# Kernel optimization log

Hardware: AMD Instinct MI355X
Metric: run time of the kernel (lower is better)

Reference implementation:

```python
import jax, jax.numpy as jnp
import numpy as np

B, T, D, U = 64, 512, 512, 512  # units must equal input feature dim (concat along axis -2)


def setup_inputs() -> dict:
    key = jax.random.key(0)
    ks = jax.random.split(key, 5)
    glorot = float(np.sqrt(2.0 / (D + U)))  # glorot_normal std
    x = jax.random.normal(ks[0], (B, T, D), dtype=jnp.float32)
    Wq = jax.random.normal(ks[1], (D, U), dtype=jnp.float32) * glorot
    Wk = jax.random.normal(ks[2], (D, U), dtype=jnp.float32) * glorot
    Wv = jax.random.normal(ks[3], (D, U), dtype=jnp.float32) * glorot
    Wrec = jax.random.normal(ks[4], (U, U), dtype=jnp.float32) * glorot
    return {"x": x, "Wq": Wq, "Wk": Wk, "Wv": Wv, "Wrec": Wrec}


def reference(x, Wq, Wk, Wv, Wrec):
    # Self_RNN forward (inference: dropout mask == ones).
    # Recurrent step over time:
    #   hist = h @ Wrec ; inp3 = stack([hist, prev_input, x_t]) -> (B,3,D)
    #   Q,K,V = inp3 @ {Wq,Wk,Wv}                              -> (B,3,U)
    #   keras batch_dot(key^T, query, axes=[1,2]) => scores[b,i,j] = K[b,i]·Q[b,j]
    #   softmax over j (the query axis); output row i=0 only:
    #   out = sum_j softmax_j(K[b,0]·Q[b,j]/sqrt(U)) * V[b,j]
    #   new states: (out, x_t).  K.rnn -> return last output.
    units = Wq.shape[1]
    scale = 1.0 / jnp.sqrt(jnp.asarray(units, x.dtype))

    def step(carry, x_t):
        h, prev = carry
        hist = h @ Wrec                               # (B,U)
        inp3 = jnp.stack([hist, prev, x_t], axis=1)   # (B,3,D)
        Q = inp3 @ Wq                                 # (B,3,U)
        K0 = inp3[:, 0] @ Wk                          # only key row 0 (hist) is used
        V = inp3 @ Wv                                 # (B,3,U)
        scores = jnp.einsum('bu,bju->bj', K0, Q) * scale   # (B,3)
        attn = jax.nn.softmax(scores, axis=-1)
        out = jnp.einsum('bj,bju->bu', attn, V)       # (B,U)
        return (out, x_t), None

    h0 = jnp.zeros((x.shape[0], units), x.dtype)
    p0 = jnp.zeros((x.shape[0], x.shape[-1]), x.dtype)
    (h_last, _), _ = jax.lax.scan(step, (h0, p0), jnp.swapaxes(x, 0, 1))
    return h_last
```

## Files before the change

### kernel.cpp

```cpp
#include <hip/hip_runtime.h>


typedef _Float16 f16;
typedef _Float16 half8 __attribute__((ext_vector_type(8)));
typedef _Float16 h2 __attribute__((ext_vector_type(2)));
typedef float floatx4 __attribute__((ext_vector_type(4)));
typedef unsigned long long u64;

#define AM_F32 0
#define AM_F16 1
#define BM_NN_F32 0
#define BM_BT_F16 1
#define BM_BT_F32 2

#if defined(__has_builtin)
#if __has_builtin(__builtin_amdgcn_fdot2)
#define HAS_FDOT2 1
#endif
#endif

__device__ inline float dot2f(h2 a, h2 b, float c) {
#ifdef HAS_FDOT2
  return __builtin_amdgcn_fdot2(a, b, c, false);
#else
  return c + (float)a[0] * (float)b[0] + (float)a[1] * (float)b[1];
#endif
}

template<int AMODE, int BMODE, int CT>
__global__ __launch_bounds__(256)
void gemm128(const void* __restrict__ Ap, const void* __restrict__ Bp,
             f16* __restrict__ C, int K, int ldbnn, long ldc, long coff,
             int ntiles) {
  __shared__ f16 Al[128 * 32];
  __shared__ f16 Bl[128 * 32];
  const int tid = threadIdx.x;
  const int lane = tid & 63;
  const int wid = tid >> 6;
  const int wr = wid >> 1, wc = wid & 1;
  const int mt = blockIdx.x / ntiles, nt = blockIdx.x % ntiles;
  const long m0 = (long)mt * 128, n0 = (long)nt * 128;

  floatx4 acc[4][4];
#pragma unroll
  for (int m = 0; m < 4; ++m)
#pragma unroll
    for (int n = 0; n < 4; ++n) acc[m][n] = (floatx4){0.f, 0.f, 0.f, 0.f};

  for (int k0 = 0; k0 < K; k0 += 32) {
    __syncthreads();
#pragma unroll
    for (int i = 0; i < 2; ++i) {
      const int slot = i * 256 + tid;
      const int row = slot >> 2;
      const int kc = (slot & 3) * 8;
      if constexpr (AMODE == AM_F16) {
        const f16* Ag = (const f16*)Ap;
        half8 v = *(const half8*)(Ag + (m0 + row) * (long)K + k0 + kc);
        *(half8*)(Al + slot * 8) = v;
      } else {
        const float* Ag = (const float*)Ap;
        const float* p = Ag + (m0 + row) * (long)K + k0 + kc;
        float4 v0 = *(const float4*)(p);
        float4 v1 = *(const float4*)(p + 4);
        half8 h;
        h[0] = (f16)v0.x; h[1] = (f16)v0.y; h[2] = (f16)v0.z; h[3] = (f16)v0.w;
        h[4] = (f16)v1.x; h[5] = (f16)v1.y; h[6] = (f16)v1.z; h[7] = (f16)v1.w;
        *(half8*)(Al + slot * 8) = h;
      }
    }
    if constexpr (BMODE == BM_NN_F32) {
      const float* Bg = (const float*)Bp;
      const int nn = tid & 127;
      const int kh = (tid >> 7) * 16;
#pragma unroll
      for (int j = 0; j < 16; j += 2) {
        float b0 = Bg[(long)(k0 + kh + j) * ldbnn + n0 + nn];
        float b1 = Bg[(long)(k0 + kh + j + 1) * ldbnn + n0 + nn];
        h2 hv; hv[0] = (f16)b0; hv[1] = (f16)b1;
        *(h2*)(Bl + nn * 32 + kh + j) = hv;
      }
    } else {
#pragma unroll
      for (int i = 0; i < 2; ++i) {
        const int slot = i * 256 + tid;
        const int row = slot >> 2;
        const int kc = (slot & 3) * 8;
        if constexpr (BMODE == BM_BT_F16) {
          const f16* Bg = (const f16*)Bp;
          half8 v = *(const half8*)(Bg + (n0 + row) * (long)K + k0 + kc);
          *(half8*)(Bl + slot * 8) = v;
        } else {
          const float* Bg = (const float*)Bp;
          const float* p = Bg + (n0 + row) * (long)K + k0 + kc;
          float4 v0 = *(const float4*)(p);
          float4 v1 = *(const float4*)(p + 4);
          half8 h;
          h[0] = (f16)v0.x; h[1] = (f16)v0.y; h[2] = (f16)v0.z; h[3] = (f16)v0.w;
          h[4] = (f16)v1.x; h[5] = (f16)v1.y; h[6] = (f16)v1.z; h[7] = (f16)v1.w;
          *(half8*)(Bl + slot * 8) = h;
        }
      }
    }
    __syncthreads();
    const int frow = lane & 15;
    const int fkc = (lane >> 4) * 8;
    half8 af[4], bf[4];
#pragma unroll
    for (int m = 0; m < 4; ++m)
      af[m] = *(const half8*)(Al + (wr * 64 + m * 16 + frow) * 32 + fkc);
#pragma unroll
    for (int n = 0; n < 4; ++n)
      bf[n] = *(const half8*)(Bl + (wc * 64 + n * 16 + frow) * 32 + fkc);
#pragma unroll
    for (int m = 0; m < 4; ++m)
#pragma unroll
      for (int n = 0; n < 4; ++n)
        acc[m][n] = __builtin_amdgcn_mfma_f32_16x16x32_f16(af[m], bf[n],
                                                           acc[m][n], 0, 0, 0);
  }
  const int crow = (lane >> 4) * 4;
  const int ccol = lane & 15;
#pragma unroll
  for (int m = 0; m < 4; ++m)
#pragma unroll
    for (int n = 0; n < 4; ++n)
#pragma unroll
      for (int r = 0; r < 4; ++r) {
        long row = m0 + wr * 64 + m * 16 + crow + r;
        long col = n0 + wc * 64 + n * 16 + ccol;
        if constexpr (CT)
          C[(coff + col) * ldc + row] = (f16)acc[m][n][r];
        else
          C[row * ldc + coff + col] = (f16)acc[m][n][r];
      }
}

__global__ void zero_ybuf(u64* ybuf) {
  ybuf[(size_t)blockIdx.x * 256 + threadIdx.x] = 0ull;
}

__global__ __launch_bounds__(256, 1)
void seq_kernel(const f16* __restrict__ Wt, const f16* __restrict__ GXV,
                u64* __restrict__ ybuf, float* __restrict__ out) {
  const int wg = blockIdx.x;
  const int grp = wg & 15;
  const int s = wg >> 4;
  const int tid = threadIdx.x;
  const int T = 512;

  __shared__ __align__(16) char wlds[64 * 1024];
  __shared__ float yred[16][4][68];
  __shared__ h2 hpk[4][256];
  __shared__ float swred[4][8];
  __shared__ float svals[4];

  {
    const int r = tid >> 2;
    const int cb = (tid & 3) * 256;
    const unsigned key = ((unsigned)(r >> 2) & 7u) << 4;
    const f16* src = Wt + (size_t)(s * 64 + r) * 512;
#pragma unroll
    for (int k = 0; k < 16; ++k) {
      half8 v = *(const half8*)((const char*)src + cb + k * 16);
      *(half8*)(wlds + r * 1024 + ((unsigned)(cb + k * 16) ^ key)) = v;
    }
  }
  {
    h2 z; z[0] = (f16)0.f; z[1] = (f16)0.f;
#pragma unroll
    for (int ch = 0; ch < 4; ++ch) hpk[ch][tid] = z;
  }
  __syncthreads();

  const int cg = tid & 15;
  const int p = tid >> 4;
  const unsigned cgx = ((unsigned)cg & 7u) << 4;
  const float scale = 0.04419417382415922f;
  const bool isV = (s < 8);
  u64* const yV = ybuf;
  u64* const s0p = ybuf + 65536;

  for (int t = 0; t < T; ++t) {
    const int par = t & 1;
    const u64 tagw = ((u64)(unsigned)(t + 1)) << 32;

    h2 gc4[4], gp4[4], xc4[4], xp4[4];
#pragma unroll
    for (int ch = 0; ch < 4; ++ch) {
      const f16* rowc = GXV + (((size_t)grp * 4 + ch) * T + t) * 1024;
      gc4[ch] = *(const h2*)(rowc + 2 * tid);
      xc4[ch] = *(const h2*)(rowc + 512 + 2 * tid);
      h2 z; z[0] = (f16)0.f; z[1] = (f16)0.f;
      gp4[ch] = z; xp4[ch] = z;
      if (t > 0) {
        gp4[ch] = *(const h2*)(rowc - 1024 + 2 * tid);
        xp4[ch] = *(const h2*)(rowc - 512 + 2 * tid);
      }
    }

    half8 ha[4][4];
#pragma unroll
    for (int g = 0; g < 4; ++g)
#pragma unroll
      for (int k4 = 0; k4 < 4; ++k4)
        ha[g][k4] = *(const half8*)&hpk[g][p * 16 + k4 * 4];
    float acc[4][4];
#pragma unroll
    for (int j = 0; j < 4; ++j)
#pragma unroll
      for (int g = 0; g < 4; ++g) acc[j][g] = 0.f;
#pragma unroll
    for (int j = 0; j < 4; ++j) {
      const char* rowb = wlds + (cg * 4 + j) * 1024;
#pragma unroll
      for (int k4 = 0; k4 < 4; ++k4) {
        half8 w = *(const half8*)(rowb + ((unsigned)(p * 64 + k4 * 16) ^ cgx));
#pragma unroll
        for (int e = 0; e < 4; ++e) {
          h2 wp; wp[0] = w[2 * e]; wp[1] = w[2 * e + 1];
#pragma unroll
          for (int g = 0; g < 4; ++g) {
            h2 hp; hp[0] = ha[g][k4][2 * e]; hp[1] = ha[g][k4][2 * e + 1];
            acc[j][g] = dot2f(wp, hp, acc[j][g]);
          }
        }
      }
    }
#pragma unroll
    for (int j = 0; j < 4; ++j)
#pragma unroll
      for (int g = 0; g < 4; ++g) yred[p][g][cg * 4 + j] = acc[j][g];
    __syncthreads();

    {
      const int ch = tid >> 6, c = tid & 63;
      float sum = 0.f;
#pragma unroll
      for (int p16 = 0; p16 < 16; ++p16) sum += yred[p16][ch][c];
      if (isV) {
        u64* dst = yV + (((size_t)grp * 2 + par) * 4 + ch) * 512 + s * 64 + c;
        __hip_atomic_store(dst, tagw | (u64)__float_as_uint(sum),
                           __ATOMIC_RELAXED, __HIP_MEMORY_SCOPE_AGENT);
      } else {
        const int u = (s - 8) * 64 + c;
        h2 hu = hpk[ch][u >> 1];
        float p0 = sum * (float)hu[u & 1];
#pragma unroll
        for (int off = 32; off > 0; off >>= 1) p0 += __shfl_down(p0, off);
        if (c == 0) {
          u64* dst = s0p + (((size_t)grp * 2 + par) * 4 + ch) * 8 + (s - 8);
          __hip_atomic_store(dst, tagw | (u64)__float_as_uint(p0),
                             __ATOMIC_RELAXED, __HIP_MEMORY_SCOPE_AGENT);
        }
      }
    }

    {
      float pr[8];
#pragma unroll
      for (int ch = 0; ch < 4; ++ch) {
        h2 hv = hpk[ch][tid];
        pr[2 * ch] = (float)gp4[ch][0] * (float)hv[0] +
                     (float)gp4[ch][1] * (float)hv[1];
        pr[2 * ch + 1] = (float)gc4[ch][0] * (float)hv[0] +
                         (float)gc4[ch][1] * (float)hv[1];
      }
#pragma unroll
      for (int off = 32; off > 0; off >>= 1)
#pragma unroll
        for (int i = 0; i < 8; ++i) pr[i] += __shfl_down(pr[i], off);
      if ((tid & 63) == 0) {
#pragma unroll
        for (int i = 0; i < 8; ++i) swred[tid >> 6][i] = pr[i];
      }
    }

    const u64* yb = yV + (((size_t)grp * 2 + par) * 4) * 512;
    const u64* s0a = s0p + (((size_t)grp * 2 + par) * 4 + ((tid >> 3) & 3)) * 8 +
                     (tid & 7);
    u64 wv[8];
    u64 w8 = tagw;
    for (;;) {
      bool ok = true;
#pragma unroll
      for (int ch = 0; ch < 4; ++ch) {
        wv[2 * ch] = __hip_atomic_load(yb + ch * 512 + 2 * tid,
                                       __ATOMIC_RELAXED, __HIP_MEMORY_SCOPE_AGENT);
        wv[2 * ch + 1] = __hip_atomic_load(yb + ch * 512 + 2 * tid + 1,
                                           __ATOMIC_RELAXED, __HIP_MEMORY_SCOPE_AGENT);
        ok = ok && (wv[2 * ch] >= tagw) && (wv[2 * ch + 1] >= tagw);
      }
      if (tid < 32) {
        w8 = __hip_atomic_load(s0a, __ATOMIC_RELAXED, __HIP_MEMORY_SCOPE_AGENT);
        ok = ok && (w8 >= tagw);
      }
      if (ok) break;
      __builtin_amdgcn_s_sleep(1);
    }

    if (tid < 32) {
      float sp = __uint_as_float((unsigned)w8);
      sp += __shfl_xor(sp, 1);
      sp += __shfl_xor(sp, 2);
      sp += __shfl_xor(sp, 4);
      if ((tid & 7) == 0) svals[tid >> 3] = sp;
    }
    __syncthreads();

#pragma unroll
    for (int ch = 0; ch < 4; ++ch) {
      float s0 = svals[ch] * scale;
      float s1 = (swred[0][2 * ch] + swred[1][2 * ch] + swred[2][2 * ch] +
                  swred[3][2 * ch]) * scale;
      float s2 = (swred[0][2 * ch + 1] + swred[1][2 * ch + 1] +
                  swred[2][2 * ch + 1] + swred[3][2 * ch + 1]) * scale;
      float mx = fmaxf(s0, fmaxf(s1, s2));
      float e0 = __expf(s0 - mx), e1 = __expf(s1 - mx), e2 = __expf(s2 - mx);
      float inv = 1.f / (e0 + e1 + e2);
      float a0 = e0 * inv, a1 = e1 * inv, a2 = e2 * inv;
      float v0 = __uint_as_float((unsigned)wv[2 * ch]);
      float v1 = __uint_as_float((unsigned)wv[2 * ch + 1]);
      float hn0 = a0 * v0 + a1 * (float)xp4[ch][0] + a2 * (float)xc4[ch][0];
      float hn1 = a0 * v1 + a1 * (float)xp4[ch][1] + a2 * (float)xc4[ch][1];
      h2 hn; hn[0] = (f16)hn0; hn[1] = (f16)hn1;
      hpk[ch][tid] = hn;
      if (t == T - 1 && s == 0) {
        out[((size_t)grp * 4 + ch) * 512 + 2 * tid] = hn0;
        out[((size_t)grp * 4 + ch) * 512 + 2 * tid + 1] = hn1;
      }
    }
    __syncthreads();
  }
}

extern "C" void kernel_launch(void* const* d_in, const int* in_sizes, int n_in,
                              void* d_out, int out_size, void* d_ws,
                              size_t ws_size, hipStream_t stream) {
  const float* x = (const float*)d_in[0];
  const float* Wq = (const float*)d_in[1];
  const float* Wk = (const float*)d_in[2];
  const float* Wv = (const float*)d_in[3];
  const float* Wrec = (const float*)d_in[4];
  float* out = (float*)d_out;

  char* ws = (char*)d_ws;
  f16* GXV = (f16*)ws;
  f16* Wt = (f16*)(ws + 67108864);
  f16* Wrk = (f16*)(ws + 68157440);
  f16* Wrq = (f16*)(ws + 68681728);
  f16* WgT = (f16*)(ws + 69206016);
  u64* ybuf = (u64*)(ws + 68681728);

  gemm128<AM_F32, BM_NN_F32, 0><<<16, 256, 0, stream>>>(Wrec, Wk, Wrk, 512, 512, 512, 0, 4);
  gemm128<AM_F32, BM_NN_F32, 0><<<16, 256, 0, stream>>>(Wrec, Wq, Wrq, 512, 512, 512, 0, 4);
  gemm128<AM_F32, BM_NN_F32, 1><<<16, 256, 0, stream>>>(Wrec, Wv, Wt, 512, 512, 512, 0, 4);
  gemm128<AM_F16, BM_BT_F16, 1><<<16, 256, 0, stream>>>(Wrk, Wrq, Wt, 512, 0, 512, 512, 4);
  gemm128<AM_F16, BM_BT_F32, 0><<<16, 256, 0, stream>>>(Wrk, Wq, WgT, 512, 0, 512, 0, 4);
  gemm128<AM_F32, BM_BT_F16, 0><<<1024, 256, 0, stream>>>(x, WgT, GXV, 512, 0, 1024, 0, 4);
  gemm128<AM_F32, BM_NN_F32, 0><<<1024, 256, 0, stream>>>(x, Wv, GXV, 512, 512, 1024, 512, 4);

  zero_ybuf<<<260, 256, 0, stream>>>(ybuf);

  const f16* WtC = Wt; const f16* GXVC = GXV;
  void* args[] = {(void*)&WtC, (void*)&GXVC, (void*)&ybuf, (void*)&out};
  dim3 grid(256), block(256);
  if (hipLaunchCooperativeKernel((const void*)seq_kernel, grid, block, args, 0,
                                 stream) != hipSuccess) {
    seq_kernel<<<grid, block, 0, stream>>>(WtC, GXVC, ybuf, out);
  }
}
```

Before: 1.890 ms.

## Use MFMA for recurrent matvec with 8-batch groups and packed f16 exchange

Reworks the persistent sequential kernel so each workgroup owns 32 output columns for 8 batch rows instead of 64 columns for 4, and computes the per-step h·W product with MFMA 16x16x32 f16 instead of scalar dot2 loops. The V results are packed two f16 values per tagged 64-bit slot, which halves the cross-workgroup exchange traffic. The s1/s2 score dot products move onto dedicated waves that read the hidden state from a swizzled LDS buffer. This targets the per-timestep compute and synchronisation latency, at the cost of f16 rounding on the exchanged V values and some dead leftover loops.

```diff
diff --git a/kernel.cpp b/kernel.cpp
--- a/kernel.cpp
+++ b/kernel.cpp
@@ -144,190 +144,263 @@
 void seq_kernel(const f16* __restrict__ Wt, const f16* __restrict__ GXV,
                 u64* __restrict__ ybuf, float* __restrict__ out) {
   const int wg = blockIdx.x;
-  const int grp = wg & 15;
-  const int s = wg >> 4;
+  const int g = wg & 7;
+  const int s = wg >> 3;
   const int tid = threadIdx.x;
+  const int lane = tid & 63;
+  const int wid = tid >> 6;
   const int T = 512;
 
-  __shared__ __align__(16) char wlds[64 * 1024];
-  __shared__ float yred[16][4][68];
-  __shared__ h2 hpk[4][256];
-  __shared__ float swred[4][8];
-  __shared__ float svals[4];
+  __shared__ __align__(16) char wlds[32 * 1024];
+  __shared__ __align__(16) char hpkb[16 * 1024];
+  __shared__ floatx4 yred[4][2][64];
+  __shared__ float svals12[8][2];
+  __shared__ float svals0[8];
 
   {
-    const int r = tid >> 2;
-    const int cb = (tid & 3) * 256;
-    const unsigned key = ((unsigned)(r >> 2) & 7u) << 4;
-    const f16* src = Wt + (size_t)(s * 64 + r) * 512;
-#pragma unroll
-    for (int k = 0; k < 16; ++k) {
-      half8 v = *(const half8*)((const char*)src + cb + k * 16);
-      *(half8*)(wlds + r * 1024 + ((unsigned)(cb + k * 16) ^ key)) = v;
+    const int col = tid >> 3;
+    const int seg = (tid & 7) * 128;
+    const unsigned key = ((unsigned)col & 7u) << 4;
+    const char* src = (const char*)(Wt + (size_t)(s * 32 + col) * 512);
+#pragma unroll
+    for (int jj = 0; jj < 8; ++jj) {
+      half8 v = *(const half8*)(src + seg + jj * 16);
+      *(half8*)(wlds + col * 1024 + ((unsigned)(seg + jj * 16) ^ key)) = v;
     }
   }
-  {
-    h2 z; z[0] = (f16)0.f; z[1] = (f16)0.f;
-#pragma unroll
-    for (int ch = 0; ch < 4; ++ch) hpk[ch][tid] = z;
-  }
+#pragma unroll
+  for (int i = 0; i < 4; ++i)
+    *(floatx4*)(hpkb + tid * 64 + i * 16) = (floatx4){0.f, 0.f, 0.f, 0.f};
   __syncthreads();
 
-  const int cg = tid & 15;
-  const int p = tid >> 4;
-  const unsigned cgx = ((unsigned)cg & 7u) << 4;
   const float scale = 0.04419417382415922f;
-  const bool isV = (s < 8);
-  u64* const yV = ybuf;
-  u64* const s0p = ybuf + 65536;
+  const bool isV = (s < 16);
+  const int ch_own = tid >> 5;
+  const int c0 = (tid & 31) * 16;
+  const unsigned hkey_own = ((unsigned)ch_own & 7u) << 4;
+  u64* const yVp = ybuf;
+  u64* const s0p = ybuf + 32768;
+
+  const int arow = lane & 15;
+  const unsigned akey = ((unsigned)arow & 7u) << 4;
+  const int bcol = lane & 15;
+  const unsigned bkey = ((unsigned)bcol & 7u) << 4;
+  const int koffb = wid * 256 + (lane >> 4) * 16;
 
   for (int t = 0; t < T; ++t) {
     const int par = t & 1;
     const u64 tagw = ((u64)(unsigned)(t + 1)) << 32;
 
-    h2 gc4[4], gp4[4], xc4[4], xp4[4];
-#pragma unroll
-    for (int ch = 0; ch < 4; ++ch) {
-      const f16* rowc = GXV + (((size_t)grp * 4 + ch) * T + t) * 1024;
-      gc4[ch] = *(const h2*)(rowc + 2 * tid);
-      xc4[ch] = *(const h2*)(rowc + 512 + 2 * tid);
-      h2 z; z[0] = (f16)0.f; z[1] = (f16)0.f;
-      gp4[ch] = z; xp4[ch] = z;
-      if (t > 0) {
-        gp4[ch] = *(const h2*)(rowc - 1024 + 2 * tid);
-        xp4[ch] = *(const h2*)(rowc - 512 + 2 * tid);
-      }
-    }
-
-    half8 ha[4][4];
-#pragma unroll
-    for (int g = 0; g < 4; ++g)
-#pragma unroll
-      for (int k4 = 0; k4 < 4; ++k4)
-        ha[g][k4] = *(const half8*)&hpk[g][p * 16 + k4 * 4];
-    float acc[4][4];
-#pragma unroll
-    for (int j = 0; j < 4; ++j)
-#pragma unroll
-      for (int g = 0; g < 4; ++g) acc[j][g] = 0.f;
-#pragma unroll
-    for (int j = 0; j < 4; ++j) {
-      const char* rowb = wlds + (cg * 4 + j) * 1024;
-#pragma unroll
-      for (int k4 = 0; k4 < 4; ++k4) {
-        half8 w = *(const half8*)(rowb + ((unsigned)(p * 64 + k4 * 16) ^ cgx));
-#pragma unroll
-        for (int e = 0; e < 4; ++e) {
-          h2 wp; wp[0] = w[2 * e]; wp[1] = w[2 * e + 1];
-#pragma unroll
-          for (int g = 0; g < 4; ++g) {
-            h2 hp; hp[0] = ha[g][k4][2 * e]; hp[1] = ha[g][k4][2 * e + 1];
-            acc[j][g] = dot2f(wp, hp, acc[j][g]);
+    const f16* rowc_own = GXV + (((size_t)g * 8 + ch_own) * T + t) * 1024;
+    half8 xc = *(const half8*)(rowc_own + 512 + c0);
+    half8 xp;
+#pragma unroll
+    for (int i = 0; i < 8; ++i) xp[i] = (f16)0.f;
+    if (t > 0) xp = *(const half8*)(rowc_own - 512 + c0);
+    half8 gcv[4], gpv[4];
+    int sch = 0, suseg = 0;
+    if (wid == 1 || wid == 2) {
+      sch = (wid - 1) * 4 + (lane >> 4);
+      suseg = (lane & 15) * 32;
+      const f16* rowg = GXV + (((size_t)g * 8 + sch) * T + t) * 1024;
+#pragma unroll
+      for (int w = 0; w < 4; ++w) {
+        gcv[w] = *(const half8*)(rowg + suseg + w * 8);
+#pragma unroll
+        for (int i = 0; i < 8; ++i) gpv[w][i] = (f16)0.f;
+      }
+      if (t > 0)
+#pragma unroll
+        for (int w = 0; w < 4; ++w)
+          gpv[w] = *(const half8*)(rowg - 1024 + suseg + w * 8);
+    }
+
+    floatx4 acc0 = (floatx4){0.f, 0.f, 0.f, 0.f};
+    floatx4 acc1 = (floatx4){0.f, 0.f, 0.f, 0.f};
+#pragma unroll
+    for (int ks = 0; ks < 4; ++ks) {
+      const unsigned ko = (unsigned)(koffb + ks * 64);
+      half8 a = *(const half8*)(hpkb + arow * 1024 + (ko ^ akey));
+      half8 b0 = *(const half8*)(wlds + bcol * 1024 + (ko ^ bkey));
+      half8 b1 = *(const half8*)(wlds + (16 + bcol) * 1024 + (ko ^ bkey));
+      acc0 = __builtin_amdgcn_mfma_f32_16x16x32_f16(a, b0, acc0, 0, 0, 0);
+      acc1 = __builtin_amdgcn_mfma_f32_16x16x32_f16(a, b1, acc1, 0, 0, 0);
+    }
+    yred[wid][0][lane] = acc0;
+    yred[wid][1][lane] = acc1;
+    __syncthreads();
+
+    if (wid == 0) {
+      floatx4 yf[2];
+#pragma unroll
+      for (int nt = 0; nt < 2; ++nt) {
+        floatx4 v = yred[0][nt][lane];
+#pragma unroll
+        for (int w = 1; w < 4; ++w) {
+          floatx4 u = yred[w][nt][lane];
+          v[0] += u[0]; v[1] += u[1]; v[2] += u[2]; v[3] += u[3];
+        }
+        yf[nt] = v;
+      }
+      if (isV) {
+#pragma unroll
+        for (int nt = 0; nt < 2; ++nt)
+#pragma unroll
+          for (int r = 0; r < 4; ++r) {
+            float v = yf[nt][r];
+            float pv = __shfl_xor(v, 1);
+            if (lane < 32 && !(lane & 1)) {
+              h2 pk; pk[0] = (f16)v; pk[1] = (f16)pv;
+              unsigned lo; __builtin_memcpy(&lo, &pk, 4);
+              const int ch = (lane >> 4) * 4 + r;
+              const int p = s * 16 + nt * 8 + ((lane & 15) >> 1);
+              __hip_atomic_store(
+                  yVp + (((size_t)g * 2 + par) * 8 + ch) * 256 + p,
+                  tagw | (u64)lo, __ATOMIC_RELAXED, __HIP_MEMORY_SCOPE_AGENT);
+            }
+          }
+      } else {
+        float sp[4] = {0.f, 0.f, 0.f, 0.f};
+#pragma unroll
+        for (int nt = 0; nt < 2; ++nt)
+#pragma unroll
+          for (int r = 0; r < 4; ++r) {
+            const int c = (s - 16) * 32 + nt * 16 + (lane & 15);
+            const int ch = (lane >> 4) * 4 + r;
+            const unsigned key = ((unsigned)ch & 7u) << 4;
+            f16 hv = *(const f16*)(hpkb + ch * 1024 + (((unsigned)(2 * c)) ^ key));
+            sp[r] += yf[nt][r] * (float)hv;
+          }
+#pragma unroll
+        for (int r = 0; r < 4; ++r) {
+          sp[r] += __shfl_xor(sp[r], 1);
+          sp[r] += __shfl_xor(sp[r], 2);
+          sp[r] += __shfl_xor(sp[r], 4);
+          sp[r] += __shfl_xor(sp[r], 8);
+        }
+        if (lane < 32 && (lane & 15) == 0) {
+          const int chb = (lane >> 4) * 4;
+#pragma unroll
+          for (int r = 0; r < 4; ++r) {
+            unsigned bits = __float_as_uint(sp[r]);
+            __hip_atomic_store(
+                s0p + (((size_t)g * 2 + par) * 8 + chb + r) * 16 + (s - 16),
+                tagw | (u64)bits, __ATOMIC_RELAXED, __HIP_MEMORY_SCOPE_AGENT);
           }
         }
       }
-    }
-#pragma unroll
-    for (int j = 0; j < 4; ++j)
-#pragma unroll
-      for (int g = 0; g < 4; ++g) yred[p][g][cg * 4 + j] = acc[j][g];
-    __syncthreads();
-
-    {
-      const int ch = tid >> 6, c = tid & 63;
-      float sum = 0.f;
-#pragma unroll
-      for (int p16 = 0; p16 < 16; ++p16) sum += yred[p16][ch][c];
-      if (isV) {
-        u64* dst = yV + (((size_t)grp * 2 + par) * 4 + ch) * 512 + s * 64 + c;
-        __hip_atomic_store(dst, tagw | (u64)__float_as_uint(sum),
-                           __ATOMIC_RELAXED, __HIP_MEMORY_SCOPE_AGENT);
-      } else {
-        const int u = (s - 8) * 64 + c;
-        h2 hu = hpk[ch][u >> 1];
-        float p0 = sum * (float)hu[u & 1];
-#pragma unroll
-        for (int off = 32; off > 0; off >>= 1) p0 += __shfl_down(p0, off);
-        if (c == 0) {
-          u64* dst = s0p + (((size_t)grp * 2 + par) * 4 + ch) * 8 + (s - 8);
-          __hip_atomic_store(dst, tagw | (u64)__float_as_uint(p0),
-                             __ATOMIC_RELAXED, __HIP_MEMORY_SCOPE_AGENT);
+    } else if (wid < 3) {
+      const unsigned skey = ((unsigned)sch & 7u) << 4;
+      half8 hh[4];
+#pragma unroll
+      for (int w = 0; w < 4; ++w)
+        hh[w] = *(const half8*)(hpkb + sch * 1024 +
+                                (((unsigned)(suseg * 2 + w * 16)) ^ skey));
+      float s1a = 0.f, s2a = 0.f;
+#pragma unroll
+      for (int w = 0; w < 4; ++w)
+#pragma unroll
+        for (int e = 0; e < 4; ++e) {
+          h2 hp; hp[0] = hh[w][2 * e]; hp[1] = hh[w][2 * e + 1];
+          h2 gp_; gp_[0] = gpv[w][2 * e]; gp_[1] = gpv[w][2 * e + 1];
+          h2 gc_; gc_[0] = gcv[w][2 * e]; gc_[1] = gcv[w][2 * e + 1];
+          s1a = dot2f(gp_, hp, s1a);
+          s2a = dot2f(gc_, hp, s2a);
         }
-      }
-    }
-
-    {
-      float pr[8];
-#pragma unroll
-      for (int ch = 0; ch < 4; ++ch) {
-        h2 hv = hpk[ch][tid];
-        pr[2 * ch] = (float)gp4[ch][0] * (float)hv[0] +
-                     (float)gp4[ch][1] * (float)hv[1];
-        pr[2 * ch + 1] = (float)gc4[ch][0] * (float)hv[0] +
-                         (float)gc4[ch][1] * (float)hv[1];
-      }
-#pragma unroll
-      for (int off = 32; off > 0; off >>= 1)
-#pragma unroll
-        for (int i = 0; i < 8; ++i) pr[i] += __shfl_down(pr[i], off);
-      if ((tid & 63) == 0) {
-#pragma unroll
-        for (int i = 0; i < 8; ++i) swred[tid >> 6][i] = pr[i];
-      }
-    }
-
-    const u64* yb = yV + (((size_t)grp * 2 + par) * 4) * 512;
-    const u64* s0a = s0p + (((size_t)grp * 2 + par) * 4 + ((tid >> 3) & 3)) * 8 +
-                     (tid & 7);
-    u64 wv[8];
-    u64 w8 = tagw;
+      s1a += __shfl_xor(s1a, 1); s2a += __shfl_xor(s2a, 1);
+      s1a += __shfl_xor(s1a, 2); s2a += __shfl_xor(s2a, 2);
+      s1a += __shfl_xor(s1a, 4); s2a += __shfl_xor(s2a, 4);
+      s1a += __shfl_xor(s1a, 8); s2a += __shfl_xor(s2a, 8);
+      if ((lane & 15) == 0) {
+        svals12[sch][0] = s1a;
+        svals12[sch][1] = s2a;
+      }
+    }
+
+    const u64* ybase =
+        yVp + (((size_t)g * 2 + par) * 8 + ch_own) * 256 + (tid & 31) * 8;
+    const u64* s0addr =
+        s0p + (((size_t)g * 2 + par) * 8 + (tid >> 4)) * 16 + (tid & 15);
+    u64 pw[8];
+    u64 s0w = tagw;
     for (;;) {
       bool ok = true;
 #pragma unroll
-      for (int ch = 0; ch < 4; ++ch) {
-        wv[2 * ch] = __hip_atomic_load(yb + ch * 512 + 2 * tid,
-                                       __ATOMIC_RELAXED, __HIP_MEMORY_SCOPE_AGENT);
-        wv[2 * ch + 1] = __hip_atomic_load(yb + ch * 512 + 2 * tid + 1,
-                                           __ATOMIC_RELAXED, __HIP_MEMORY_SCOPE_AGENT);
-        ok = ok && (wv[2 * ch] >= tagw) && (wv[2 * ch + 1] >= tagw);
-      }
-      if (tid < 32) {
-        w8 = __hip_atomic_load(s0a, __ATOMIC_RELAXED, __HIP_MEMORY_SCOPE_AGENT);
-        ok = ok && (w8 >= tagw);
+      for (int i = 0; i < 8; ++i) {
+        pw[i] = __hip_atomic_load(ybase + i, __ATOMIC_RELAXED,
+                                  __HIP_MEMORY_SCOPE_AGENT);
+        ok = ok && (pw[i] >= tagw);
+      }
+      if (tid < 128) {
+        s0w = __hip_atomic_load(s0addr, __ATOMIC_RELAXED,
+                                __HIP_MEMORY_SCOPE_AGENT);
+        ok = ok && (s0w >= tagw);
       }
       if (ok) break;
       __builtin_amdgcn_s_sleep(1);
     }
 
-    if (tid < 32) {
-      float sp = __uint_as_float((unsigned)w8);
+    if (tid < 128) {
+      float sp = __uint_as_float((unsigned)s0w);
       sp += __shfl_xor(sp, 1);
       sp += __shfl_xor(sp, 2);
       sp += __shfl_xor(sp, 4);
-      if ((tid & 7) == 0) svals[tid >> 3] = sp;
+      sp += __shfl_xor(sp, 8);
+      if ((lane & 15) == 0) svals0[tid >> 4] = sp;
     }
     __syncthreads();
 
-#pragma unroll
-    for (int ch = 0; ch < 4; ++ch) {
-      float s0 = svals[ch] * scale;
-      float s1 = (swred[0][2 * ch] + swred[1][2 * ch] + swred[2][2 * ch] +
-                  swred[3][2 * ch]) * scale;
-      float s2 = (swred[0][2 * ch + 1] + swred[1][2 * ch + 1] +
-                  swred[2][2 * ch + 1] + swred[3][2 * ch + 1]) * scale;
-      float mx = fmaxf(s0, fmaxf(s1, s2));
-      float e0 = __expf(s0 - mx), e1 = __expf(s1 - mx), e2 = __expf(s2 - mx);
+    {
+      float s0v = svals0[ch_own] * scale;
+      float s1v = svals12[ch_own][0] * scale;
+      float s2v = svals12[ch_own][1] * scale;
+      float mx = fmaxf(s0v, fmaxf(s1v, s2v));
+      float e0 = __expf(s0v - mx), e1 = __expf(s1v - mx), e2 = __expf(s2v - mx);
       float inv = 1.f / (e0 + e1 + e2);
       float a0 = e0 * inv, a1 = e1 * inv, a2 = e2 * inv;
-      float v0 = __uint_as_float((unsigned)wv[2 * ch]);
-      float v1 = __uint_as_float((unsigned)wv[2 * ch + 1]);
-      float hn0 = a0 * v0 + a1 * (float)xp4[ch][0] + a2 * (float)xc4[ch][0];
-      float hn1 = a0 * v1 + a1 * (float)xp4[ch][1] + a2 * (float)xc4[ch][1];
-      h2 hn; hn[0] = (f16)hn0; hn[1] = (f16)hn1;
-      hpk[ch][tid] = hn;
+      half8 hna, hnb;
+#pragma unroll
+      for (int i = 0; i < 8; ++i) {
+        unsigned lo = (unsigned)pw[i];
+        h2 vh; __builtin_memcpy(&vh, &lo, 4);
+        float f0 = a0 * (float)vh[0] + a1 * (float)xp[i] + a2 * (float)xc[i];
+        (void)f0;
+      }
+      float hnf[16];
+#pragma unroll
+      for (int i = 0; i < 8; ++i) {
+        unsigned lo = (unsigned)pw[i];
+        h2 vh; __builtin_memcpy(&vh, &lo, 4);
+        const int j0 = 2 * i, j1 = 2 * i + 1;
+        float xpc0 = (j0 < 8) ? (float)xp[j0] : (float)xp[j0 - 8];
+        (void)xpc0;
+        hnf[j0] = 0.f; hnf[j1] = 0.f;
+      }
+      half8 xc2 = *(const half8*)(rowc_own + 512 + c0 + 8);
+      half8 xp2;
+#pragma unroll
+      for (int i = 0; i < 8; ++i) xp2[i] = (f16)0.f;
+      if (t > 0) xp2 = *(const half8*)(rowc_own - 512 + c0 + 8);
+#pragma unroll
+      for (int i = 0; i < 8; ++i) {
+        unsigned lo = (unsigned)pw[i];
+        h2 vh; __builtin_memcpy(&vh, &lo, 4);
+        const int j0 = 2 * i, j1 = 2 * i + 1;
+        float xcj0 = (j0 < 8) ? (float)xc[j0] : (float)xc2[j0 - 8];
+        float xcj1 = (j1 < 8) ? (float)xc[j1] : (float)xc2[j1 - 8];
+        float xpj0 = (j0 < 8) ? (float)xp[j0] : (float)xp2[j0 - 8];
+        float xpj1 = (j1 < 8) ? (float)xp[j1] : (float)xp2[j1 - 8];
+        hnf[j0] = a0 * (float)vh[0] + a1 * xpj0 + a2 * xcj0;
+        hnf[j1] = a0 * (float)vh[1] + a1 * xpj1 + a2 * xcj1;
+      }
+#pragma unroll
+      for (int j = 0; j < 8; ++j) { hna[j] = (f16)hnf[j]; hnb[j] = (f16)hnf[j + 8]; }
+      *(half8*)(hpkb + ch_own * 1024 + (((unsigned)(2 * c0)) ^ hkey_own)) = hna;
+      *(half8*)(hpkb + ch_own * 1024 + (((unsigned)(2 * c0 + 16)) ^ hkey_own)) = hnb;
       if (t == T - 1 && s == 0) {
-        out[((size_t)grp * 4 + ch) * 512 + 2 * tid] = hn0;
-        out[((size_t)grp * 4 + ch) * 512 + 2 * tid + 1] = hn1;
+        float* ob = out + ((size_t)g * 8 + ch_own) * 512 + c0;
+#pragma unroll
+        for (int j = 0; j < 16; ++j) ob[j] = hnf[j];
       }
     }
     __syncthreads();
@@ -360,7 +433,7 @@
   gemm128<AM_F32, BM_BT_F16, 0><<<1024, 256, 0, stream>>>(x, WgT, GXV, 512, 0, 1024, 0, 4);
   gemm128<AM_F32, BM_NN_F32, 0><<<1024, 256, 0, stream>>>(x, Wv, GXV, 512, 512, 1024, 512, 4);
 
-  zero_ybuf<<<260, 256, 0, stream>>>(ybuf);
+  zero_ybuf<<<136, 256, 0, stream>>>(ybuf);
 
   const f16* WtC = Wt; const f16* GXVC = GXV;
   void* args[] = {(void*)&WtC, (void*)&GXVC, (void*)&ybuf, (void*)&out};
```

New measurement: 3.336 ms. 1.76x slower.

## Use MFMA for per-step recurrent matvec and pack exchanged values as fp16 pairs

Applied to the files above, without the earlier changes.

Replaces the per-step fdot2 dot-product loops in the persistent recurrent kernel with 16x16x32 f16 MFMA instructions over a swizzled LDS hidden-state tile, and shrinks the cross-reduction to four waves. The V values exchanged between workgroups are now packed as two fp16 halves per tagged 64-bit word, which halves the global flag buffer. Each thread now owns eight contiguous hidden elements of one batch row, so one LDS sync per step is removed. The intent is to cut per-step compute and synchronisation latency on the serial critical path, at the cost of extra fp16 rounding on the exchanged values.

```diff
diff --git a/kernel.cpp b/kernel.cpp
--- a/kernel.cpp
+++ b/kernel.cpp
@@ -147,187 +147,179 @@
   const int grp = wg & 15;
   const int s = wg >> 4;
   const int tid = threadIdx.x;
+  const int lane = tid & 63;
+  const int wid = tid >> 6;
   const int T = 512;
 
   __shared__ __align__(16) char wlds[64 * 1024];
-  __shared__ float yred[16][4][68];
-  __shared__ h2 hpk[4][256];
+  __shared__ __align__(16) char hpkb[16 * 1024];
+  __shared__ floatx4 yred[4][4][16];
   __shared__ float swred[4][8];
-  __shared__ float svals[4];
 
   {
-    const int r = tid >> 2;
-    const int cb = (tid & 3) * 256;
-    const unsigned key = ((unsigned)(r >> 2) & 7u) << 4;
-    const f16* src = Wt + (size_t)(s * 64 + r) * 512;
+    const int col = tid >> 2;
+    const int seg = (tid & 3) * 256;
+    const unsigned key = ((unsigned)col & 7u) << 4;
+    const char* src = (const char*)(Wt + (size_t)(s * 64 + col) * 512);
 #pragma unroll
     for (int k = 0; k < 16; ++k) {
-      half8 v = *(const half8*)((const char*)src + cb + k * 16);
-      *(half8*)(wlds + r * 1024 + ((unsigned)(cb + k * 16) ^ key)) = v;
+      half8 v = *(const half8*)(src + seg + k * 16);
+      *(half8*)(wlds + col * 1024 + ((unsigned)(seg + k * 16) ^ key)) = v;
     }
   }
-  {
-    h2 z; z[0] = (f16)0.f; z[1] = (f16)0.f;
-#pragma unroll
-    for (int ch = 0; ch < 4; ++ch) hpk[ch][tid] = z;
-  }
+#pragma unroll
+  for (int i = 0; i < 4; ++i)
+    *(floatx4*)(hpkb + tid * 64 + i * 16) = (floatx4){0.f, 0.f, 0.f, 0.f};
   __syncthreads();
 
-  const int cg = tid & 15;
-  const int p = tid >> 4;
-  const unsigned cgx = ((unsigned)cg & 7u) << 4;
   const float scale = 0.04419417382415922f;
   const bool isV = (s < 8);
-  u64* const yV = ybuf;
-  u64* const s0p = ybuf + 65536;
+  const int ch = tid >> 6;
+  const int lc = tid & 63;
+  const int cb = lc * 8;
+  const unsigned hkey = ((unsigned)ch) << 4;
+  u64* const yVp = ybuf;
+  u64* const s0p = ybuf + 32768;
+
+  const int arow = lane & 15;
+  const unsigned abkey = ((unsigned)(arow & 7)) << 4;
+  const int kbase = wid * 256 + (lane >> 4) * 16;
 
   for (int t = 0; t < T; ++t) {
     const int par = t & 1;
     const u64 tagw = ((u64)(unsigned)(t + 1)) << 32;
 
-    h2 gc4[4], gp4[4], xc4[4], xp4[4];
-#pragma unroll
-    for (int ch = 0; ch < 4; ++ch) {
-      const f16* rowc = GXV + (((size_t)grp * 4 + ch) * T + t) * 1024;
-      gc4[ch] = *(const h2*)(rowc + 2 * tid);
-      xc4[ch] = *(const h2*)(rowc + 512 + 2 * tid);
+    const f16* rowc = GXV + (((size_t)grp * 4 + ch) * T + t) * 1024;
+    half8 xc = *(const half8*)(rowc + 512 + cb);
+    half8 xp;
+#pragma unroll
+    for (int i = 0; i < 8; ++i) xp[i] = (f16)0.f;
+    if (t > 0) xp = *(const half8*)(rowc - 512 + cb);
+    h2 gcv[4], gpv[4];
+#pragma unroll
+    for (int c4 = 0; c4 < 4; ++c4) {
+      const f16* rg = GXV + (((size_t)grp * 4 + c4) * T + t) * 1024;
+      gcv[c4] = *(const h2*)(rg + 2 * tid);
       h2 z; z[0] = (f16)0.f; z[1] = (f16)0.f;
-      gp4[ch] = z; xp4[ch] = z;
-      if (t > 0) {
-        gp4[ch] = *(const h2*)(rowc - 1024 + 2 * tid);
-        xp4[ch] = *(const h2*)(rowc - 512 + 2 * tid);
-      }
-    }
-
-    half8 ha[4][4];
-#pragma unroll
-    for (int g = 0; g < 4; ++g)
-#pragma unroll
-      for (int k4 = 0; k4 < 4; ++k4)
-        ha[g][k4] = *(const half8*)&hpk[g][p * 16 + k4 * 4];
-    float acc[4][4];
-#pragma unroll
-    for (int j = 0; j < 4; ++j)
-#pragma unroll
-      for (int g = 0; g < 4; ++g) acc[j][g] = 0.f;
-#pragma unroll
-    for (int j = 0; j < 4; ++j) {
-      const char* rowb = wlds + (cg * 4 + j) * 1024;
-#pragma unroll
-      for (int k4 = 0; k4 < 4; ++k4) {
-        half8 w = *(const half8*)(rowb + ((unsigned)(p * 64 + k4 * 16) ^ cgx));
-#pragma unroll
-        for (int e = 0; e < 4; ++e) {
-          h2 wp; wp[0] = w[2 * e]; wp[1] = w[2 * e + 1];
-#pragma unroll
-          for (int g = 0; g < 4; ++g) {
-            h2 hp; hp[0] = ha[g][k4][2 * e]; hp[1] = ha[g][k4][2 * e + 1];
-            acc[j][g] = dot2f(wp, hp, acc[j][g]);
-          }
-        }
-      }
-    }
-#pragma unroll
-    for (int j = 0; j < 4; ++j)
-#pragma unroll
-      for (int g = 0; g < 4; ++g) yred[p][g][cg * 4 + j] = acc[j][g];
-    __syncthreads();
-
-    {
-      const int ch = tid >> 6, c = tid & 63;
-      float sum = 0.f;
-#pragma unroll
-      for (int p16 = 0; p16 < 16; ++p16) sum += yred[p16][ch][c];
-      if (isV) {
-        u64* dst = yV + (((size_t)grp * 2 + par) * 4 + ch) * 512 + s * 64 + c;
-        __hip_atomic_store(dst, tagw | (u64)__float_as_uint(sum),
-                           __ATOMIC_RELAXED, __HIP_MEMORY_SCOPE_AGENT);
-      } else {
-        const int u = (s - 8) * 64 + c;
-        h2 hu = hpk[ch][u >> 1];
-        float p0 = sum * (float)hu[u & 1];
-#pragma unroll
-        for (int off = 32; off > 0; off >>= 1) p0 += __shfl_down(p0, off);
-        if (c == 0) {
-          u64* dst = s0p + (((size_t)grp * 2 + par) * 4 + ch) * 8 + (s - 8);
-          __hip_atomic_store(dst, tagw | (u64)__float_as_uint(p0),
-                             __ATOMIC_RELAXED, __HIP_MEMORY_SCOPE_AGENT);
-        }
+      gpv[c4] = z;
+      if (t > 0) gpv[c4] = *(const h2*)(rg - 1024 + 2 * tid);
+    }
+
+    floatx4 acc[4];
+#pragma unroll
+    for (int nt = 0; nt < 4; ++nt) acc[nt] = (floatx4){0.f, 0.f, 0.f, 0.f};
+#pragma unroll
+    for (int i = 0; i < 4; ++i) {
+      const unsigned ko = (unsigned)(kbase + i * 64);
+      half8 av = *(const half8*)(hpkb + arow * 1024 + (ko ^ abkey));
+#pragma unroll
+      for (int nt = 0; nt < 4; ++nt) {
+        half8 bv = *(const half8*)(wlds + (nt * 16 + arow) * 1024 + (ko ^ abkey));
+        acc[nt] = __builtin_amdgcn_mfma_f32_16x16x32_f16(av, bv, acc[nt], 0, 0, 0);
       }
     }
 
     {
       float pr[8];
 #pragma unroll
-      for (int ch = 0; ch < 4; ++ch) {
-        h2 hv = hpk[ch][tid];
-        pr[2 * ch] = (float)gp4[ch][0] * (float)hv[0] +
-                     (float)gp4[ch][1] * (float)hv[1];
-        pr[2 * ch + 1] = (float)gc4[ch][0] * (float)hv[0] +
-                         (float)gc4[ch][1] * (float)hv[1];
+      for (int c4 = 0; c4 < 4; ++c4) {
+        h2 hv = *(const h2*)(hpkb + c4 * 1024 +
+                             (((unsigned)(4 * tid)) ^ (((unsigned)c4) << 4)));
+        pr[2 * c4] = dot2f(gpv[c4], hv, 0.f);
+        pr[2 * c4 + 1] = dot2f(gcv[c4], hv, 0.f);
       }
 #pragma unroll
       for (int off = 32; off > 0; off >>= 1)
 #pragma unroll
         for (int i = 0; i < 8; ++i) pr[i] += __shfl_down(pr[i], off);
-      if ((tid & 63) == 0) {
-#pragma unroll
-        for (int i = 0; i < 8; ++i) swred[tid >> 6][i] = pr[i];
-      }
-    }
-
-    const u64* yb = yV + (((size_t)grp * 2 + par) * 4) * 512;
-    const u64* s0a = s0p + (((size_t)grp * 2 + par) * 4 + ((tid >> 3) & 3)) * 8 +
-                     (tid & 7);
-    u64 wv[8];
-    u64 w8 = tagw;
+      if (lane == 0) {
+#pragma unroll
+        for (int i = 0; i < 8; ++i) swred[wid][i] = pr[i];
+      }
+    }
+
+    if (lane < 16) {
+#pragma unroll
+      for (int nt = 0; nt < 4; ++nt) yred[wid][nt][lane] = acc[nt];
+    }
+    __syncthreads();
+
+    {
+      const int nt = lc >> 4, l15 = lc & 15;
+      float y = 0.f;
+#pragma unroll
+      for (int w = 0; w < 4; ++w)
+        y += ((const float*)&yred[w][nt][l15])[ch];
+      if (isV) {
+        float yp = __shfl_xor(y, 1);
+        if (!(lane & 1)) {
+          h2 pk; pk[0] = (f16)y; pk[1] = (f16)yp;
+          unsigned lo; __builtin_memcpy(&lo, &pk, 4);
+          __hip_atomic_store(
+              yVp + (((size_t)grp * 2 + par) * 4 + ch) * 256 + s * 32 + (lc >> 1),
+              tagw | (u64)lo, __ATOMIC_RELAXED, __HIP_MEMORY_SCOPE_AGENT);
+        }
+      } else {
+        const int u = (s - 8) * 64 + lc;
+        f16 hu = *(const f16*)(hpkb + ch * 1024 + (((unsigned)(2 * u)) ^ hkey));
+        float p = y * (float)hu;
+#pragma unroll
+        for (int off = 32; off > 0; off >>= 1) p += __shfl_down(p, off);
+        if (lane == 0)
+          __hip_atomic_store(
+              s0p + (((size_t)grp * 2 + par) * 4 + ch) * 8 + (s - 8),
+              tagw | (u64)__float_as_uint(p), __ATOMIC_RELAXED,
+              __HIP_MEMORY_SCOPE_AGENT);
+      }
+    }
+
+    const u64* vb = yVp + (((size_t)grp * 2 + par) * 4 + ch) * 256 + lc * 4;
+    const u64* sb = s0p + (((size_t)grp * 2 + par) * 4 + ch) * 8 + (tid & 7);
+    u64 v0, v1, v2, v3, sw;
     for (;;) {
-      bool ok = true;
-#pragma unroll
-      for (int ch = 0; ch < 4; ++ch) {
-        wv[2 * ch] = __hip_atomic_load(yb + ch * 512 + 2 * tid,
-                                       __ATOMIC_RELAXED, __HIP_MEMORY_SCOPE_AGENT);
-        wv[2 * ch + 1] = __hip_atomic_load(yb + ch * 512 + 2 * tid + 1,
-                                           __ATOMIC_RELAXED, __HIP_MEMORY_SCOPE_AGENT);
-        ok = ok && (wv[2 * ch] >= tagw) && (wv[2 * ch + 1] >= tagw);
-      }
-      if (tid < 32) {
-        w8 = __hip_atomic_load(s0a, __ATOMIC_RELAXED, __HIP_MEMORY_SCOPE_AGENT);
-        ok = ok && (w8 >= tagw);
-      }
-      if (ok) break;
+      v0 = __hip_atomic_load(vb + 0, __ATOMIC_RELAXED, __HIP_MEMORY_SCOPE_AGENT);
+      v1 = __hip_atomic_load(vb + 1, __ATOMIC_RELAXED, __HIP_MEMORY_SCOPE_AGENT);
+      v2 = __hip_atomic_load(vb + 2, __ATOMIC_RELAXED, __HIP_MEMORY_SCOPE_AGENT);
+      v3 = __hip_atomic_load(vb + 3, __ATOMIC_RELAXED, __HIP_MEMORY_SCOPE_AGENT);
+      sw = __hip_atomic_load(sb, __ATOMIC_RELAXED, __HIP_MEMORY_SCOPE_AGENT);
+      if (v0 >= tagw && v1 >= tagw && v2 >= tagw && v3 >= tagw && sw >= tagw)
+        break;
       __builtin_amdgcn_s_sleep(1);
     }
 
-    if (tid < 32) {
-      float sp = __uint_as_float((unsigned)w8);
-      sp += __shfl_xor(sp, 1);
-      sp += __shfl_xor(sp, 2);
-      sp += __shfl_xor(sp, 4);
-      if ((tid & 7) == 0) svals[tid >> 3] = sp;
-    }
-    __syncthreads();
-
-#pragma unroll
-    for (int ch = 0; ch < 4; ++ch) {
-      float s0 = svals[ch] * scale;
-      float s1 = (swred[0][2 * ch] + swred[1][2 * ch] + swred[2][2 * ch] +
-                  swred[3][2 * ch]) * scale;
-      float s2 = (swred[0][2 * ch + 1] + swred[1][2 * ch + 1] +
-                  swred[2][2 * ch + 1] + swred[3][2 * ch + 1]) * scale;
-      float mx = fmaxf(s0, fmaxf(s1, s2));
-      float e0 = __expf(s0 - mx), e1 = __expf(s1 - mx), e2 = __expf(s2 - mx);
-      float inv = 1.f / (e0 + e1 + e2);
-      float a0 = e0 * inv, a1 = e1 * inv, a2 = e2 * inv;
-      float v0 = __uint_as_float((unsigned)wv[2 * ch]);
-      float v1 = __uint_as_float((unsigned)wv[2 * ch + 1]);
-      float hn0 = a0 * v0 + a1 * (float)xp4[ch][0] + a2 * (float)xc4[ch][0];
-      float hn1 = a0 * v1 + a1 * (float)xp4[ch][1] + a2 * (float)xc4[ch][1];
-      h2 hn; hn[0] = (f16)hn0; hn[1] = (f16)hn1;
-      hpk[ch][tid] = hn;
+    float sp = __uint_as_float((unsigned)sw);
+    sp += __shfl_xor(sp, 1);
+    sp += __shfl_xor(sp, 2);
+    sp += __shfl_xor(sp, 4);
+    const float sv0 = sp * scale;
+    const float sv1 = (swred[0][2 * ch] + swred[1][2 * ch] + swred[2][2 * ch] +
+                       swred[3][2 * ch]) * scale;
+    const float sv2 = (swred[0][2 * ch + 1] + swred[1][2 * ch + 1] +
+                       swred[2][2 * ch + 1] + swred[3][2 * ch + 1]) * scale;
+    const float mx = fmaxf(sv0, fmaxf(sv1, sv2));
+    const float e0 = __expf(sv0 - mx), e1 = __expf(sv1 - mx), e2 = __expf(sv2 - mx);
+    const float inv = 1.f / (e0 + e1 + e2);
+    const float a0 = e0 * inv, a1 = e1 * inv, a2 = e2 * inv;
+
+    {
+      float hnf[8];
+      u64 vw[4] = {v0, v1, v2, v3};
+#pragma unroll
+      for (int i = 0; i < 4; ++i) {
+        unsigned lo = (unsigned)vw[i];
+        h2 vh; __builtin_memcpy(&vh, &lo, 4);
+        hnf[2 * i] = a0 * (float)vh[0] + a1 * (float)xp[2 * i] + a2 * (float)xc[2 * i];
+        hnf[2 * i + 1] = a0 * (float)vh[1] + a1 * (float)xp[2 * i + 1] +
+                         a2 * (float)xc[2 * i + 1];
+      }
+      half8 hn;
+#pragma unroll
+      for (int j = 0; j < 8; ++j) hn[j] = (f16)hnf[j];
+      *(half8*)(hpkb + ch * 1024 + (((unsigned)(2 * cb)) ^ hkey)) = hn;
       if (t == T - 1 && s == 0) {
-        out[((size_t)grp * 4 + ch) * 512 + 2 * tid] = hn0;
-        out[((size_t)grp * 4 + ch) * 512 + 2 * tid + 1] = hn1;
+        float* ob = out + ((size_t)grp * 4 + ch) * 512 + cb;
+#pragma unroll
+        for (int j = 0; j < 8; ++j) ob[j] = hnf[j];
       }
     }
     __syncthreads();
@@ -360,7 +352,7 @@
   gemm128<AM_F32, BM_BT_F16, 0><<<1024, 256, 0, stream>>>(x, WgT, GXV, 512, 0, 1024, 0, 4);
   gemm128<AM_F32, BM_NN_F32, 0><<<1024, 256, 0, stream>>>(x, Wv, GXV, 512, 512, 1024, 512, 4);
 
-  zero_ybuf<<<260, 256, 0, stream>>>(ybuf);
+  zero_ybuf<<<132, 256, 0, stream>>>(ybuf);
 
   const f16* WtC = Wt; const f16* GXVC = GXV;
   void* args[] = {(void*)&WtC, (void*)&GXVC, (void*)&ybuf, (void*)&out};
```

After: 2.155 ms. 14.0% more time.
